# Performance work log

Measured on AMD Instinct MI355X. Metric: run time of the kernel, lower is better.

The kernel has to match this reference:

```python
import jax, jax.numpy as jnp
import numpy as np

B, L, T = 128, 64, 48
E, H, V_SRC, V_TGT = 512, 512, 32000, 32000
NEG = -1e9


def lstm_cell(x, h, c, Wih, Whh, b):
    g = x @ Wih.T + h @ Whh.T + b
    i, f, gg, o = jnp.split(g, 4, axis=-1)
    c2 = jax.nn.sigmoid(f) * c + jax.nn.sigmoid(i) * jnp.tanh(gg)
    return jax.nn.sigmoid(o) * jnp.tanh(c2), c2


def setup_inputs() -> dict:
    key = jax.random.key(0)
    ks = jax.random.split(key, 24)
    s = 0.02
    src_tokens = jax.random.randint(ks[0], (B, L), 0, V_SRC)
    trg_tokens = jax.random.randint(ks[1], (B, T), 0, V_TGT)
    # packed-sequence semantics require descending src_lens; max must equal L
    src_lens = jnp.sort(jax.random.randint(ks[2], (B,), L // 2, L + 1))[::-1].at[0].set(L)
    trg_lens = jnp.sort(jax.random.randint(ks[3], (B,), T // 2, T + 1))[::-1].at[0].set(T)
    p = lambda k, shp: (jax.random.normal(k, shp, dtype=jnp.float32) * s)
    return {
        'src_tokens': src_tokens, 'src_lens': src_lens,
        'trg_tokens': trg_tokens, 'trg_lens': trg_lens,
        'src_emb': p(ks[4], (V_SRC, E)), 'trg_emb': p(ks[5], (V_TGT, E)),
        'enc_Wih0': p(ks[6], (4 * H, E)), 'enc_Whh0': p(ks[7], (4 * H, H)), 'enc_b0': p(ks[8], (4 * H,)),
        'enc_Wih1': p(ks[9], (4 * H, H)), 'enc_Whh1': p(ks[10], (4 * H, H)), 'enc_b1': p(ks[11], (4 * H,)),
        'dec_Wih': p(ks[12], (4 * H, E + H)), 'dec_Whh': p(ks[13], (4 * H, H)), 'dec_b': p(ks[14], (4 * H,)),
        'hid_W': p(ks[15], (H, 2 * H)), 'hid_b': p(ks[16], (H,)),
        'out_W': p(ks[17], (V_TGT, H)), 'out_b': p(ks[18], (V_TGT,)),
        'init_W': p(ks[19], (H, 2 * H)), 'init_b': p(ks[20], (H,)),
    }


def reference(src_tokens, src_lens, trg_tokens, trg_lens,
              src_emb, trg_emb,
              enc_Wih0, enc_Whh0, enc_b0, enc_Wih1, enc_Whh1, enc_b1,
              dec_Wih, dec_Whh, dec_b,
              hid_W, hid_b, out_W, out_b, init_W, init_b):
    # ---- encode (2-layer LSTM with packed-sequence semantics; dropout in eval = identity) ----
    x = src_emb[src_tokens]                                   # (B, L, E)
    xs = jnp.swapaxes(x, 0, 1)                                # (L, B, E)
    step_mask = (jnp.arange(L)[:, None] < src_lens[None, :])[..., None]  # (L, B, 1)
    z = jnp.zeros((B, H), dtype=x.dtype)

    def enc_step(carry, inp):
        h1, c1, h2, c2 = carry
        x_t, m = inp
        nh1, nc1 = lstm_cell(x_t, h1, c1, enc_Wih0, enc_Whh0, enc_b0)
        nh2, nc2 = lstm_cell(nh1, h2, c2, enc_Wih1, enc_Whh1, enc_b1)
        h1 = jnp.where(m, nh1, h1); c1 = jnp.where(m, nc1, c1)
        h2 = jnp.where(m, nh2, h2); c2 = jnp.where(m, nc2, c2)
        return (h1, c1, h2, c2), jnp.where(m, nh2, 0.0)

    (h1, c1, h2, c2), outs = jax.lax.scan(enc_step, (z, z, z, z), (xs, step_mask))
    src_states = jnp.swapaxes(outs, 0, 1)                     # (B, L, H), zero-padded
    final_cell = jnp.concatenate([c1, c2], axis=-1)           # (B, 2H) = layers flattened
    c0 = final_cell @ init_W.T + init_b
    h0 = jnp.tanh(c0)

    # ---- decode (teacher forcing; dot-product attention masked by src_lens) ----
    src_pos_mask = jnp.arange(L)[None, :] < src_lens[:, None]  # (B, L)
    toks = jnp.swapaxes(trg_tokens[:, :-1], 0, 1)              # (T-1, B)
    tgts = jnp.swapaxes(trg_tokens[:, 1:], 0, 1)               # (T-1, B)

    def dec_step(carry, inp):
        h, c, av = carry
        tok, tgt = inp
        v = trg_emb[tok]                                       # (B, E)
        h, c = lstm_cell(jnp.concatenate([v, av], -1), h, c, dec_Wih, dec_Whh, dec_b)
        scores = jnp.einsum('bh,blh->bl', h, src_states)
        scores = jnp.where(src_pos_mask, scores, NEG)
        attn = jax.nn.softmax(scores, axis=-1)
        ctx = jnp.einsum('bl,blh->bh', attn, src_states)
        av = jnp.concatenate([h, ctx], -1) @ hid_W.T + hid_b
        logits = av @ out_W.T + out_b                          # (B, V_TGT)
        logp = jax.nn.log_softmax(logits, axis=-1)
        nll = -jnp.take_along_axis(logp, tgt[:, None], axis=-1)[:, 0]
        return (h, c, av), nll

    _, nll = jax.lax.scan(dec_step, (h0, c0, z), (toks, tgts))
    nll = jnp.swapaxes(nll, 0, 1)                              # (B, T-1)
    mask = (jnp.arange(T)[None, :] < trg_lens[:, None]).astype(nll.dtype)
    return jnp.sum(-nll * mask[:, 1:])
```

## Files before the change

### kernel.cpp

```cpp
#include <hip/hip_runtime.h>
#include <hip/hip_bf16.h>
#include <math.h>

typedef __bf16 bf16;
typedef __bf16 bf16x8 __attribute__((ext_vector_type(8)));
typedef float  f32x4  __attribute__((ext_vector_type(4)));

#define MFMA16(a,b,c) __builtin_amdgcn_mfma_f32_16x16x32_bf16(a,b,c,0,0,0)

namespace {

constexpr int Bn = 128, Ln = 64, Tn = 48, En = 512, Hn = 512, Vn = 32000;
constexpr int G4 = 2048;
constexpr int TD = Tn - 1;
constexpr int MD = TD * Bn;
constexpr float NEGV = -1e9f;
constexpr int HB = Bn * Hn;

__device__ __forceinline__ float sigm(float x){ return 1.f/(1.f+__expf(-x)); }

__global__ void k_conv(const float4* __restrict__ s, ushort4* __restrict__ d, int n4){
  int i = blockIdx.x*256 + threadIdx.x;
  if (i >= n4) return;
  float4 v = s[i];
  union { bf16 h[4]; ushort4 u; } pk;
  pk.h[0]=(bf16)v.x; pk.h[1]=(bf16)v.y; pk.h[2]=(bf16)v.z; pk.h[3]=(bf16)v.w;
  d[i] = pk.u;
}

__global__ void k_gather_src(const int* __restrict__ toks, const float* __restrict__ emb,
                             ushort4* __restrict__ Xe){
  int i = blockIdx.x*256 + threadIdx.x;
  int e4 = i & (En/4 - 1);
  int r  = i >> 7;
  int l = r >> 7, b = r & (Bn-1);
  int tok = toks[b*Ln + l];
  float4 v = *(const float4*)(emb + (size_t)tok*En + e4*4);
  union { bf16 h[4]; ushort4 u; } pk;
  pk.h[0]=(bf16)v.x; pk.h[1]=(bf16)v.y; pk.h[2]=(bf16)v.z; pk.h[3]=(bf16)v.w;
  Xe[i] = pk.u;
}

__global__ void k_gather_trg(const int* __restrict__ toks, const float* __restrict__ emb,
                             ushort4* __restrict__ Vg){
  int i = blockIdx.x*256 + threadIdx.x;
  int e4 = i & (En/4 - 1);
  int r  = i >> 7;
  int t = r >> 7, b = r & (Bn-1);
  int tok = toks[b*Tn + t];
  float4 v = *(const float4*)(emb + (size_t)tok*En + e4*4);
  union { bf16 h[4]; ushort4 u; } pk;
  pk.h[0]=(bf16)v.x; pk.h[1]=(bf16)v.y; pk.h[2]=(bf16)v.z; pk.h[3]=(bf16)v.w;
  Vg[i] = pk.u;
}

__global__ void k_zero(bf16* __restrict__ a, bf16* __restrict__ b,
                       float* __restrict__ c, float* __restrict__ d,
                       float* __restrict__ outp){
  int i = blockIdx.x*256 + threadIdx.x;
  a[i] = (bf16)0.f; b[i] = (bf16)0.f; c[i] = 0.f; d[i] = 0.f;
  if (i == 0) outp[0] = 0.f;
}

template<int MODE>
__global__ void __launch_bounds__(512) k_gemm(
    const bf16* __restrict__ A, const bf16* __restrict__ Bw,
    const float* __restrict__ bias, void* __restrict__ Ovp,
    float* __restrict__ pmax, float* __restrict__ psum,
    int Ncols, int Mrows)
{
  constexpr int K = 512;
  int lane = threadIdx.x & 63, w = threadIdx.x >> 6;
  int wr = w & 3, wc = w >> 2;
  int mt = blockIdx.x, nt = blockIdx.y;
  int mBase = mt*128 + wr*32;
  int nBase = nt*256 + wc*128;
  int laneK = (lane >> 4) * 8;
  const bf16* Ap = A  + (size_t)(mBase + (lane&15))*K + laneK;
  const bf16* Bp = Bw + (size_t)(nBase + (lane&15))*K + laneK;
  f32x4 acc[2][8] = {};
  for (int kb = 0; kb < K; kb += 32){
    bf16x8 a0 = *(const bf16x8*)(Ap + kb);
    bf16x8 a1 = *(const bf16x8*)(Ap + (size_t)16*K + kb);
    #pragma unroll
    for (int fn = 0; fn < 8; ++fn){
      bf16x8 bv = *(const bf16x8*)(Bp + (size_t)fn*16*K + kb);
      acc[0][fn] = MFMA16(a0, bv, acc[0][fn]);
      acc[1][fn] = MFMA16(a1, bv, acc[1][fn]);
    }
  }
  float bvv[8];
  #pragma unroll
  for (int fn = 0; fn < 8; ++fn) bvv[fn] = bias[nBase + fn*16 + (lane&15)];

  if constexpr (MODE == 0){
    bf16* O = (bf16*)Ovp;
    #pragma unroll
    for (int fm = 0; fm < 2; ++fm){
      #pragma unroll
      for (int r = 0; r < 4; ++r){
        size_t ro = (size_t)(mBase + fm*16 + ((lane>>4)<<2) + r) * Ncols;
        #pragma unroll
        for (int fn = 0; fn < 8; ++fn)
          O[ro + nBase + fn*16 + (lane&15)] = (bf16)(acc[fm][fn][r] + bvv[fn]);
      }
    }
  } else {
    int pc = nt*2 + wc;
    #pragma unroll
    for (int fm = 0; fm < 2; ++fm){
      #pragma unroll
      for (int r = 0; r < 4; ++r){
        float mx = -1e30f;
        #pragma unroll
        for (int fn = 0; fn < 8; ++fn) mx = fmaxf(mx, acc[fm][fn][r] + bvv[fn]);
        mx = fmaxf(mx, __shfl_xor(mx, 1));
        mx = fmaxf(mx, __shfl_xor(mx, 2));
        mx = fmaxf(mx, __shfl_xor(mx, 4));
        mx = fmaxf(mx, __shfl_xor(mx, 8));
        float sm = 0.f;
        #pragma unroll
        for (int fn = 0; fn < 8; ++fn) sm += __expf(acc[fm][fn][r] + bvv[fn] - mx);
        sm += __shfl_xor(sm, 1); sm += __shfl_xor(sm, 2);
        sm += __shfl_xor(sm, 4); sm += __shfl_xor(sm, 8);
        if ((lane & 15) == 0){
          int row = mBase + fm*16 + ((lane>>4)<<2) + r;
          pmax[(size_t)pc*Mrows + row] = mx;
          psum[(size_t)pc*Mrows + row] = sm;
        }
      }
    }
  }
}

__device__ __forceinline__ void kloop4(f32x4 acc[4], const bf16* __restrict__ Ap,
                                       const bf16* __restrict__ Wp, int ldw, int col)
{
  for (int kb = 0; kb < 512; kb += 32){
    bf16x8 a = *(const bf16x8*)(Ap + kb);
    #pragma unroll
    for (int q = 0; q < 4; ++q){
      bf16x8 bv = *(const bf16x8*)(Wp + (size_t)(q*Hn + col)*ldw + kb);
      acc[q] = MFMA16(a, bv, acc[q]);
    }
  }
}

__global__ void __launch_bounds__(256) k_enc(
    const bf16* __restrict__ Xg,
    bf16* __restrict__ h1b, bf16* __restrict__ h2b,
    float* __restrict__ c1, float* __restrict__ c2,
    const bf16* __restrict__ Whh0, const bf16* __restrict__ Wih1,
    const bf16* __restrict__ Whh1, const float* __restrict__ b1,
    const int* __restrict__ slens, bf16* __restrict__ Sst, int t)
{
  int bx = blockIdx.x;
  int lane = threadIdx.x & 63, w = threadIdx.x >> 6;
  bool isE2 = bx >= 64;
  int bb = isE2 ? bx - 64 : bx;
  int mt = bb >> 3, cg = bb & 7;
  int col  = cg*64 + w*16 + (lane & 15);
  int rowA = mt*16 + (lane & 15);
  int rowC = mt*16 + ((lane >> 4) << 2);
  int laneK = (lane >> 4) * 8;
  int rb = t & 1;

  if (!isE2){
    if (t >= Ln) return;
    f32x4 acc[4];
    #pragma unroll
    for (int q = 0; q < 4; ++q){
      #pragma unroll
      for (int r = 0; r < 4; ++r)
        acc[q][r] = (float)Xg[((size_t)(t*Bn + rowC + r))*G4 + q*Hn + col];
    }
    kloop4(acc, h1b + rb*HB + rowA*Hn + laneK, Whh0 + laneK, Hn, col);
    #pragma unroll
    for (int r = 0; r < 4; ++r){
      int grow = rowC + r;
      float cold = c1[grow*Hn + col];
      float iv = sigm(acc[0][r]), fv = sigm(acc[1][r]);
      float gv = tanhf(acc[2][r]), ov = sigm(acc[3][r]);
      float cn = fv*cold + iv*gv;
      float hn = ov*tanhf(cn);
      bool m = t < slens[grow];
      float hold = (float)h1b[rb*HB + grow*Hn + col];
      c1[grow*Hn + col] = m ? cn : cold;
      h1b[(rb^1)*HB + grow*Hn + col] = (bf16)(m ? hn : hold);
    }
  } else {
    int t2 = t - 1;
    if (t2 < 0) return;
    f32x4 acc[4];
    #pragma unroll
    for (int q = 0; q < 4; ++q){
      float bq = b1[q*Hn + col];
      #pragma unroll
      for (int r = 0; r < 4; ++r) acc[q][r] = bq;
    }
    kloop4(acc, h1b + rb*HB + rowA*Hn + laneK, Wih1 + laneK, Hn, col);
    kloop4(acc, h2b + rb*HB + rowA*Hn + laneK, Whh1 + laneK, Hn, col);
    #pragma unroll
    for (int r = 0; r < 4; ++r){
      int grow = rowC + r;
      float cold = c2[grow*Hn + col];
      float iv = sigm(acc[0][r]), fv = sigm(acc[1][r]);
      float gv = tanhf(acc[2][r]), ov = sigm(acc[3][r]);
      float cn = fv*cold + iv*gv;
      float hn = ov*tanhf(cn);
      bool m = t2 < slens[grow];
      float hold = (float)h2b[rb*HB + grow*Hn + col];
      c2[grow*Hn + col] = m ? cn : cold;
      h2b[(rb^1)*HB + grow*Hn + col] = (bf16)(m ? hn : hold);
      Sst[((size_t)grow*Ln + t2)*Hn + col] = m ? (bf16)hn : (bf16)0.f;
    }
  }
}

__global__ void k_dec_init(const float* __restrict__ c1, const float* __restrict__ c2,
                           const float* __restrict__ iW, const float* __restrict__ ib,
                           float* __restrict__ cd, bf16* __restrict__ hdb)
{
  int n = blockIdx.x;
  int b = threadIdx.x;
  float s = ib[n];
  const float* w0 = iW + (size_t)n*(2*Hn);
  for (int k = 0; k < Hn; ++k) s += c1[b*Hn + k] * w0[k];
  for (int k = 0; k < Hn; ++k) s += c2[b*Hn + k] * w0[Hn + k];
  cd[b*Hn + n] = s;
  hdb[b*Hn + n] = (bf16)tanhf(s);
}

__global__ void __launch_bounds__(256) k_dec1(
    const bf16* __restrict__ Vg, const bf16* __restrict__ av_all,
    bf16* __restrict__ hdb, float* __restrict__ cd,
    const bf16* __restrict__ Wdih, const bf16* __restrict__ Wdhh,
    const float* __restrict__ db, int t)
{
  int bb = blockIdx.x;
  int lane = threadIdx.x & 63, w = threadIdx.x >> 6;
  int mt = bb >> 3, cg = bb & 7;
  int col  = cg*64 + w*16 + (lane & 15);
  int rowA = mt*16 + (lane & 15);
  int rowC = mt*16 + ((lane >> 4) << 2);
  int laneK = (lane >> 4) * 8;
  int rb = t & 1;
  f32x4 acc[4];
  #pragma unroll
  for (int q = 0; q < 4; ++q){
    float bq = db[q*Hn + col];
    #pragma unroll
    for (int r = 0; r < 4; ++r) acc[q][r] = bq;
  }
  kloop4(acc, Vg + (size_t)t*Bn*En + rowA*En + laneK, Wdih + laneK, En+Hn, col);
  if (t > 0)
    kloop4(acc, av_all + (size_t)(t-1)*HB + rowA*Hn + laneK, Wdih + En + laneK, En+Hn, col);
  kloop4(acc, hdb + rb*HB + rowA*Hn + laneK, Wdhh + laneK, Hn, col);
  #pragma unroll
  for (int r = 0; r < 4; ++r){
    int grow = rowC + r;
    float cold = cd[grow*Hn + col];
    float iv = sigm(acc[0][r]), fv = sigm(acc[1][r]);
    float gv = tanhf(acc[2][r]), ov = sigm(acc[3][r]);
    float cn = fv*cold + iv*gv;
    float hn = ov*tanhf(cn);
    cd[grow*Hn + col] = cn;
    hdb[(rb^1)*HB + grow*Hn + col] = (bf16)hn;
  }
}

__global__ void __launch_bounds__(256) k_attn(
    const bf16* __restrict__ hdb, const bf16* __restrict__ Sst,
    const int* __restrict__ slens, bf16* __restrict__ ctx, int t)
{
  int b = blockIdx.x, tid = threadIdx.x;
  const bf16* h = hdb + ((t&1)^1)*HB + (size_t)b*Hn;
  const bf16* S = Sst + (size_t)b*Ln*Hn;
  __shared__ float sc[Ln];
  __shared__ float at[Ln];
  int l = tid >> 2, kq = tid & 3;
  float s = 0.f;
  {
    const bf16* hp = h + kq*128;
    const bf16* Sp = S + (size_t)l*Hn + kq*128;
    for (int k8 = 0; k8 < 128; k8 += 8){
      bf16x8 hv = *(const bf16x8*)(hp + k8);
      bf16x8 sv = *(const bf16x8*)(Sp + k8);
      #pragma unroll
      for (int j = 0; j < 8; ++j) s += (float)hv[j]*(float)sv[j];
    }
  }
  s += __shfl_xor(s, 1); s += __shfl_xor(s, 2);
  if (kq == 0) sc[l] = (l < slens[b]) ? s : NEGV;
  __syncthreads();
  float mx = -1e30f;
  for (int j = 0; j < Ln; ++j) mx = fmaxf(mx, sc[j]);
  if (tid < Ln) at[tid] = __expf(sc[tid] - mx);
  __syncthreads();
  float den = 0.f;
  for (int j = 0; j < Ln; ++j) den += at[j];
  float inv = 1.f/den;
  for (int kk = tid; kk < Hn; kk += 256){
    float c = 0.f;
    for (int j = 0; j < Ln; ++j) c += at[j]*(float)S[(size_t)j*Hn + kk];
    ctx[(size_t)b*Hn + kk] = (bf16)(c*inv);
  }
}

__global__ void __launch_bounds__(256) k_hid(
    const bf16* __restrict__ hdb, const bf16* __restrict__ ctx,
    const bf16* __restrict__ Whid, const float* __restrict__ hbias,
    bf16* __restrict__ av_all, int t)
{
  int bb = blockIdx.x;
  int lane = threadIdx.x & 63, w = threadIdx.x >> 6;
  int mt = bb >> 3, cg = bb & 7;
  int col  = cg*64 + w*16 + (lane & 15);
  int rowA = mt*16 + (lane & 15);
  int rowC = mt*16 + ((lane >> 4) << 2);
  int laneK = (lane >> 4) * 8;
  int rb2 = (t & 1) ^ 1;
  float bq = hbias[col];
  f32x4 acc = {bq, bq, bq, bq};
  const bf16* Ah = hdb + rb2*HB + rowA*Hn + laneK;
  const bf16* Ac = ctx + rowA*Hn + laneK;
  const bf16* Wp = Whid + (size_t)col*(2*Hn) + laneK;
  for (int kb = 0; kb < 512; kb += 32){
    bf16x8 a  = *(const bf16x8*)(Ah + kb);
    bf16x8 bv = *(const bf16x8*)(Wp + kb);
    acc = MFMA16(a, bv, acc);
  }
  for (int kb = 0; kb < 512; kb += 32){
    bf16x8 a  = *(const bf16x8*)(Ac + kb);
    bf16x8 bv = *(const bf16x8*)(Wp + Hn + kb);
    acc = MFMA16(a, bv, acc);
  }
  #pragma unroll
  for (int r = 0; r < 4; ++r)
    av_all[(size_t)t*HB + (size_t)(rowC + r)*Hn + col] = (bf16)acc[r];
}

__global__ void k_tgt(const bf16* __restrict__ av_all, const bf16* __restrict__ Wout,
                      const float* __restrict__ ob, const int* __restrict__ trg_tokens,
                      float* __restrict__ tlog)
{
  int row = blockIdx.x*4 + (threadIdx.x >> 6);
  int lane = threadIdx.x & 63;
  int t = row >> 7, b = row & 127;
  int tok = trg_tokens[b*Tn + t + 1];
  bf16x8 va = *(const bf16x8*)(av_all + (size_t)row*Hn + lane*8);
  bf16x8 vw = *(const bf16x8*)(Wout + (size_t)tok*Hn + lane*8);
  float s = 0.f;
  #pragma unroll
  for (int j = 0; j < 8; ++j) s += (float)va[j]*(float)vw[j];
  #pragma unroll
  for (int sh = 1; sh < 64; sh <<= 1) s += __shfl_xor(s, sh);
  if (lane == 0) tlog[row] = s + ob[tok];
}

__global__ void k_lse(const float* __restrict__ pmax, const float* __restrict__ psum,
                      const float* __restrict__ tlog, const int* __restrict__ tlens,
                      float* __restrict__ out)
{
  int row = blockIdx.x*512 + threadIdx.x;
  float contrib = 0.f;
  if (row < MD){
    float mx = -1e30f;
    for (int pc = 0; pc < 250; ++pc) mx = fmaxf(mx, pmax[(size_t)pc*MD + row]);
    float s = 0.f;
    for (int pc = 0; pc < 250; ++pc)
      s += psum[(size_t)pc*MD + row] * __expf(pmax[(size_t)pc*MD + row] - mx);
    float lse = mx + __logf(s);
    int t = row >> 7, b = row & 127;
    if (t + 1 < tlens[b]) contrib = tlog[row] - lse;
  }
  #pragma unroll
  for (int sh = 1; sh < 64; sh <<= 1) contrib += __shfl_xor(contrib, sh);
  __shared__ float wsum[8];
  if ((threadIdx.x & 63) == 0) wsum[threadIdx.x >> 6] = contrib;
  __syncthreads();
  if (threadIdx.x == 0){
    float s2 = 0.f;
    for (int i = 0; i < 8; ++i) s2 += wsum[i];
    atomicAdd(out, s2);
  }
}

}

extern "C" void kernel_launch(void* const* d_in, const int* in_sizes, int n_in,
                              void* d_out, int out_size, void* d_ws, size_t ws_size,
                              hipStream_t stream)
{
  (void)in_sizes; (void)n_in; (void)out_size; (void)ws_size;
  const int*   src_tokens = (const int*)  d_in[0];
  const int*   src_lens   = (const int*)  d_in[1];
  const int*   trg_tokens = (const int*)  d_in[2];
  const int*   trg_lens   = (const int*)  d_in[3];
  const float* src_emb    = (const float*)d_in[4];
  const float* trg_emb    = (const float*)d_in[5];
  const float* eWih0 = (const float*)d_in[6];
  const float* eWhh0 = (const float*)d_in[7];
  const float* eb0   = (const float*)d_in[8];
  const float* eWih1 = (const float*)d_in[9];
  const float* eWhh1 = (const float*)d_in[10];
  const float* eb1   = (const float*)d_in[11];
  const float* dWih  = (const float*)d_in[12];
  const float* dWhh  = (const float*)d_in[13];
  const float* db    = (const float*)d_in[14];
  const float* hW    = (const float*)d_in[15];
  const float* hb    = (const float*)d_in[16];
  const float* oW    = (const float*)d_in[17];
  const float* ob    = (const float*)d_in[18];
  const float* iW    = (const float*)d_in[19];
  const float* ib    = (const float*)d_in[20];

  char* p = (char*)d_ws;
  auto alloc = [&](size_t bytes)->void*{
    void* r = (void*)p; p += (bytes + 255) & ~(size_t)255; return r;
  };
  bf16* wih0  = (bf16*)alloc((size_t)G4*En*2);
  bf16* whh0  = (bf16*)alloc((size_t)G4*Hn*2);
  bf16* wih1  = (bf16*)alloc((size_t)G4*Hn*2);
  bf16* whh1  = (bf16*)alloc((size_t)G4*Hn*2);
  bf16* wdih  = (bf16*)alloc((size_t)G4*(En+Hn)*2);
  bf16* wdhh  = (bf16*)alloc((size_t)G4*Hn*2);
  bf16* whid  = (bf16*)alloc((size_t)Hn*(2*Hn)*2);
  bf16* wout  = (bf16*)alloc((size_t)Vn*Hn*2);
  bf16* Xe    = (bf16*)alloc((size_t)Ln*Bn*En*2);
  bf16* Vg    = (bf16*)alloc((size_t)TD*Bn*En*2);
  bf16* Sst   = (bf16*)alloc((size_t)Bn*Ln*Hn*2);
  bf16* h1b   = (bf16*)alloc((size_t)2*HB*2);
  bf16* h2b   = (bf16*)alloc((size_t)2*HB*2);
  bf16* hdb   = (bf16*)alloc((size_t)2*HB*2);
  bf16* ctx   = (bf16*)alloc((size_t)HB*2);
  bf16* avall = (bf16*)alloc((size_t)TD*HB*2);
  bf16* Xg    = (bf16*)alloc((size_t)Ln*Bn*G4*2);
  float* c1   = (float*)alloc((size_t)HB*4);
  float* c2   = (float*)alloc((size_t)HB*4);
  float* cd   = (float*)alloc((size_t)HB*4);
  float* pmax = (float*)alloc((size_t)250*MD*4);
  float* psum = (float*)alloc((size_t)250*MD*4);
  float* tlog = (float*)alloc((size_t)MD*4);
  float* outp = (float*)d_out;

  auto conv = [&](const float* s, bf16* d, int n){
    int n4 = n/4;
    k_conv<<<(n4+255)/256, 256, 0, stream>>>((const float4*)s, (ushort4*)d, n4);
  };
  conv(eWih0, wih0, G4*En);
  conv(eWhh0, whh0, G4*Hn);
  conv(eWih1, wih1, G4*Hn);
  conv(eWhh1, whh1, G4*Hn);
  conv(dWih,  wdih, G4*(En+Hn));
  conv(dWhh,  wdhh, G4*Hn);
  conv(hW,    whid, Hn*2*Hn);
  conv(oW,    wout, Vn*Hn);

  k_gather_src<<<4096, 256, 0, stream>>>(src_tokens, src_emb, (ushort4*)Xe);
  k_gather_trg<<<3008, 256, 0, stream>>>(trg_tokens, trg_emb, (ushort4*)Vg);
  k_zero<<<256, 256, 0, stream>>>(h1b, h2b + HB, c1, c2, outp);

  k_gemm<0><<<dim3(64, 8), 512, 0, stream>>>(Xe, wih0, eb0, Xg, nullptr, nullptr, G4, Ln*Bn);

  for (int t = 0; t <= Ln; ++t)
    k_enc<<<128, 256, 0, stream>>>(Xg, h1b, h2b, c1, c2, whh0, wih1, whh1, eb1,
                                   src_lens, Sst, t);

  k_dec_init<<<512, 128, 0, stream>>>(c1, c2, iW, ib, cd, hdb);

  for (int t = 0; t < TD; ++t){
    k_dec1<<<64, 256, 0, stream>>>(Vg, avall, hdb, cd, wdih, wdhh, db, t);
    k_attn<<<128, 256, 0, stream>>>(hdb, Sst, src_lens, ctx, t);
    k_hid<<<64, 256, 0, stream>>>(hdb, ctx, whid, hb, avall, t);
  }

  k_tgt<<<1504, 256, 0, stream>>>(avall, wout, ob, trg_tokens, tlog);

  k_gemm<1><<<dim3(47, 125), 512, 0, stream>>>(avall, wout, ob, nullptr, pmax, psum, Vn, MD);

  k_lse<<<12, 512, 0, stream>>>(pmax, psum, tlog, trg_lens, outp);
}
```

Before: 5.282 ms.

## Persistent encoder/decoder kernels with global barriers and LDS-tiled GEMM

Replaces the per-timestep kernel launches of the encoder and decoder with two persistent kernels that loop over time and synchronise blocks through per-row-group atomic flag barriers. The recurrent GEMMs are split along K across waves and reduced in LDS, so 256 blocks are active per step instead of 64-128. The decoder's input-embedding projection is hoisted into one batched GEMM before the loop, and decoder init, attention and the hidden projection are folded in. The large GEMMs now stage tiles into swizzled LDS via global_load_lds. The spin barriers depend on all blocks being co-resident and have a timeout break that could silently desynchronise.

```diff
diff --git a/kernel.cpp b/kernel.cpp
--- a/kernel.cpp
+++ b/kernel.cpp
@@ -18,6 +18,29 @@
 constexpr int HB = Bn * Hn;
 
 __device__ __forceinline__ float sigm(float x){ return 1.f/(1.f+__expf(-x)); }
+
+__device__ __forceinline__ void gload16(const bf16* g, bf16* l){
+  __builtin_amdgcn_global_load_lds(
+    (const __attribute__((address_space(1))) void*)g,
+    (__attribute__((address_space(3))) void*)l, 16, 0, 0);
+}
+
+__device__ __forceinline__ void gbar(int* flags, int gbase, int nb, int slot, int s){
+  __builtin_amdgcn_fence(__ATOMIC_RELEASE, "agent");
+  __syncthreads();
+  if (threadIdx.x == 0)
+    __hip_atomic_store(flags + gbase + slot, s, __ATOMIC_RELAXED, __HIP_MEMORY_SCOPE_AGENT);
+  if ((int)threadIdx.x < nb){
+    int lim = 0;
+    while (__hip_atomic_load(flags + gbase + (int)threadIdx.x,
+                             __ATOMIC_RELAXED, __HIP_MEMORY_SCOPE_AGENT) < s){
+      __builtin_amdgcn_s_sleep(1);
+      if (++lim > (1<<18)) break;
+    }
+  }
+  __syncthreads();
+  __builtin_amdgcn_fence(__ATOMIC_ACQUIRE, "agent");
+}
 
 __global__ void k_conv(const float4* __restrict__ s, ushort4* __restrict__ d, int n4){
   int i = blockIdx.x*256 + threadIdx.x;
@@ -54,133 +77,197 @@
   Vg[i] = pk.u;
 }
 
-__global__ void k_zero(bf16* __restrict__ a, bf16* __restrict__ b,
-                       float* __restrict__ c, float* __restrict__ d,
+__global__ void k_zero(bf16* __restrict__ h1b0, bf16* __restrict__ h2b1,
+                       float* __restrict__ c1, float* __restrict__ c2,
+                       int* __restrict__ ef, int* __restrict__ df,
                        float* __restrict__ outp){
   int i = blockIdx.x*256 + threadIdx.x;
-  a[i] = (bf16)0.f; b[i] = (bf16)0.f; c[i] = 0.f; d[i] = 0.f;
+  h1b0[i] = (bf16)0.f; h2b1[i] = (bf16)0.f; c1[i] = 0.f; c2[i] = 0.f;
+  if (i < 256){ ef[i] = 0; df[i] = 0; }
   if (i == 0) outp[0] = 0.f;
 }
 
 template<int MODE>
-__global__ void __launch_bounds__(512) k_gemm(
-    const bf16* __restrict__ A, const bf16* __restrict__ Bw,
-    const float* __restrict__ bias, void* __restrict__ Ovp,
-    float* __restrict__ pmax, float* __restrict__ psum,
-    int Ncols, int Mrows)
+__global__ void __launch_bounds__(256) k_gemm2(
+    const bf16* __restrict__ A, int lda,
+    const bf16* __restrict__ Bw, int ldb,
+    const float* __restrict__ bias,
+    bf16* __restrict__ O, int ldo,
+    float* __restrict__ pmax, float* __restrict__ psum, int Mrows)
 {
-  constexpr int K = 512;
-  int lane = threadIdx.x & 63, w = threadIdx.x >> 6;
-  int wr = w & 3, wc = w >> 2;
-  int mt = blockIdx.x, nt = blockIdx.y;
-  int mBase = mt*128 + wr*32;
-  int nBase = nt*256 + wc*128;
-  int laneK = (lane >> 4) * 8;
-  const bf16* Ap = A  + (size_t)(mBase + (lane&15))*K + laneK;
-  const bf16* Bp = Bw + (size_t)(nBase + (lane&15))*K + laneK;
-  f32x4 acc[2][8] = {};
-  for (int kb = 0; kb < K; kb += 32){
-    bf16x8 a0 = *(const bf16x8*)(Ap + kb);
-    bf16x8 a1 = *(const bf16x8*)(Ap + (size_t)16*K + kb);
+  __shared__ bf16 As[128*64];
+  __shared__ bf16 Bs[128*64];
+  __shared__ float redm[2][64], reds[2][64];
+  int tid = threadIdx.x;
+  int lane = tid & 63, w = tid >> 6;
+  int wr = w & 1, wc = w >> 1;
+  int c15 = lane & 15, hi = lane >> 4;
+  int mBase = blockIdx.x*128, nBase = blockIdx.y*128;
+  int l8 = lane >> 3;
+  int k8 = (lane & 7) ^ l8;
+  int swz = c15 & 7;
+
+  f32x4 acc[4][4] = {};
+  int rA[4], cB[4];
+  #pragma unroll
+  for (int m = 0; m < 4; ++m) rA[m] = (wr*64 + m*16 + c15)*64;
+  #pragma unroll
+  for (int n = 0; n < 4; ++n) cB[n] = (wc*64 + n*16 + c15)*64;
+
+  for (int kt = 0; kt < 8; ++kt){
+    __syncthreads();
     #pragma unroll
-    for (int fn = 0; fn < 8; ++fn){
-      bf16x8 bv = *(const bf16x8*)(Bp + (size_t)fn*16*K + kb);
-      acc[0][fn] = MFMA16(a0, bv, acc[0][fn]);
-      acc[1][fn] = MFMA16(a1, bv, acc[1][fn]);
-    }
-  }
-  float bvv[8];
+    for (int i = 0; i < 4; ++i){
+      int s = i*4 + w;
+      int row = s*8 + l8;
+      gload16(A + (size_t)(mBase+row)*lda + kt*64 + k8*8, As + s*512);
+      gload16(Bw + (size_t)(nBase+row)*ldb + kt*64 + k8*8, Bs + s*512);
+    }
+    __syncthreads();
+    bf16x8 af[4][2], bf[4][2];
+    #pragma unroll
+    for (int m = 0; m < 4; ++m)
+      #pragma unroll
+      for (int j = 0; j < 2; ++j)
+        af[m][j] = *(const bf16x8*)(As + rA[m] + (((j*4+hi) ^ swz) << 3));
+    #pragma unroll
+    for (int n = 0; n < 4; ++n)
+      #pragma unroll
+      for (int j = 0; j < 2; ++j)
+        bf[n][j] = *(const bf16x8*)(Bs + cB[n] + (((j*4+hi) ^ swz) << 3));
+    #pragma unroll
+    for (int m = 0; m < 4; ++m)
+      #pragma unroll
+      for (int n = 0; n < 4; ++n){
+        acc[m][n] = MFMA16(af[m][0], bf[n][0], acc[m][n]);
+        acc[m][n] = MFMA16(af[m][1], bf[n][1], acc[m][n]);
+      }
+  }
+
+  float bvv[4];
   #pragma unroll
-  for (int fn = 0; fn < 8; ++fn) bvv[fn] = bias[nBase + fn*16 + (lane&15)];
+  for (int n = 0; n < 4; ++n) bvv[n] = bias[nBase + wc*64 + n*16 + c15];
 
   if constexpr (MODE == 0){
-    bf16* O = (bf16*)Ovp;
     #pragma unroll
-    for (int fm = 0; fm < 2; ++fm){
+    for (int m = 0; m < 4; ++m)
       #pragma unroll
       for (int r = 0; r < 4; ++r){
-        size_t ro = (size_t)(mBase + fm*16 + ((lane>>4)<<2) + r) * Ncols;
-        #pragma unroll
-        for (int fn = 0; fn < 8; ++fn)
-          O[ro + nBase + fn*16 + (lane&15)] = (bf16)(acc[fm][fn][r] + bvv[fn]);
-      }
-    }
+        size_t ro = (size_t)(mBase + wr*64 + m*16 + hi*4 + r) * ldo + nBase + wc*64;
+        #pragma unroll
+        for (int n = 0; n < 4; ++n)
+          O[ro + n*16 + c15] = (bf16)(acc[m][n][r] + bvv[n]);
+      }
   } else {
-    int pc = nt*2 + wc;
+    float lmx[4][4], lsm[4][4];
     #pragma unroll
-    for (int fm = 0; fm < 2; ++fm){
+    for (int m = 0; m < 4; ++m)
       #pragma unroll
       for (int r = 0; r < 4; ++r){
         float mx = -1e30f;
         #pragma unroll
-        for (int fn = 0; fn < 8; ++fn) mx = fmaxf(mx, acc[fm][fn][r] + bvv[fn]);
-        mx = fmaxf(mx, __shfl_xor(mx, 1));
-        mx = fmaxf(mx, __shfl_xor(mx, 2));
-        mx = fmaxf(mx, __shfl_xor(mx, 4));
-        mx = fmaxf(mx, __shfl_xor(mx, 8));
+        for (int n = 0; n < 4; ++n) mx = fmaxf(mx, acc[m][n][r] + bvv[n]);
+        mx = fmaxf(mx, __shfl_xor(mx,1)); mx = fmaxf(mx, __shfl_xor(mx,2));
+        mx = fmaxf(mx, __shfl_xor(mx,4)); mx = fmaxf(mx, __shfl_xor(mx,8));
         float sm = 0.f;
         #pragma unroll
-        for (int fn = 0; fn < 8; ++fn) sm += __expf(acc[fm][fn][r] + bvv[fn] - mx);
-        sm += __shfl_xor(sm, 1); sm += __shfl_xor(sm, 2);
-        sm += __shfl_xor(sm, 4); sm += __shfl_xor(sm, 8);
-        if ((lane & 15) == 0){
-          int row = mBase + fm*16 + ((lane>>4)<<2) + r;
-          pmax[(size_t)pc*Mrows + row] = mx;
-          psum[(size_t)pc*Mrows + row] = sm;
-        }
-      }
-    }
-  }
-}
-
-__device__ __forceinline__ void kloop4(f32x4 acc[4], const bf16* __restrict__ Ap,
-                                       const bf16* __restrict__ Wp, int ldw, int col)
-{
-  for (int kb = 0; kb < 512; kb += 32){
-    bf16x8 a = *(const bf16x8*)(Ap + kb);
-    #pragma unroll
-    for (int q = 0; q < 4; ++q){
-      bf16x8 bv = *(const bf16x8*)(Wp + (size_t)(q*Hn + col)*ldw + kb);
-      acc[q] = MFMA16(a, bv, acc[q]);
-    }
-  }
-}
-
-__global__ void __launch_bounds__(256) k_enc(
+        for (int n = 0; n < 4; ++n) sm += __expf(acc[m][n][r] + bvv[n] - mx);
+        sm += __shfl_xor(sm,1); sm += __shfl_xor(sm,2);
+        sm += __shfl_xor(sm,4); sm += __shfl_xor(sm,8);
+        lmx[m][r] = mx; lsm[m][r] = sm;
+        if (c15 == 0 && wc == 1){
+          int rs = m*16 + hi*4 + r;
+          redm[wr][rs] = mx; reds[wr][rs] = sm;
+        }
+      }
+    __syncthreads();
+    if (wc == 0 && c15 == 0){
+      int pc = blockIdx.y;
+      #pragma unroll
+      for (int m = 0; m < 4; ++m)
+        #pragma unroll
+        for (int r = 0; r < 4; ++r){
+          int rs = m*16 + hi*4 + r;
+          float m1 = redm[wr][rs], s1 = reds[wr][rs];
+          float M = fmaxf(lmx[m][r], m1);
+          float S = lsm[m][r]*__expf(lmx[m][r]-M) + s1*__expf(m1-M);
+          size_t o = (size_t)pc*Mrows + mBase + wr*64 + rs;
+          pmax[o] = M; psum[o] = S;
+        }
+    }
+  }
+}
+
+__global__ void __launch_bounds__(256) k_encp(
     const bf16* __restrict__ Xg,
     bf16* __restrict__ h1b, bf16* __restrict__ h2b,
     float* __restrict__ c1, float* __restrict__ c2,
     const bf16* __restrict__ Whh0, const bf16* __restrict__ Wih1,
     const bf16* __restrict__ Whh1, const float* __restrict__ b1,
-    const int* __restrict__ slens, bf16* __restrict__ Sst, int t)
+    const int* __restrict__ slens, bf16* __restrict__ Sst,
+    int* __restrict__ flags)
 {
-  int bx = blockIdx.x;
-  int lane = threadIdx.x & 63, w = threadIdx.x >> 6;
-  bool isE2 = bx >= 64;
-  int bb = isE2 ? bx - 64 : bx;
-  int mt = bb >> 3, cg = bb & 7;
-  int col  = cg*64 + w*16 + (lane & 15);
-  int rowA = mt*16 + (lane & 15);
-  int rowC = mt*16 + ((lane >> 4) << 2);
-  int laneK = (lane >> 4) * 8;
-  int rb = t & 1;
-
-  if (!isE2){
-    if (t >= Ln) return;
-    f32x4 acc[4];
-    #pragma unroll
-    for (int q = 0; q < 4; ++q){
-      #pragma unroll
-      for (int r = 0; r < 4; ++r)
-        acc[q][r] = (float)Xg[((size_t)(t*Bn + rowC + r))*G4 + q*Hn + col];
-    }
-    kloop4(acc, h1b + rb*HB + rowA*Hn + laneK, Whh0 + laneK, Hn, col);
-    #pragma unroll
-    for (int r = 0; r < 4; ++r){
-      int grow = rowC + r;
+  __shared__ float red[2][4][64][17];
+  int tid = threadIdx.x;
+  int lane = tid & 63, w = tid >> 6;
+  int c15 = lane & 15, hi = lane >> 4;
+  int rg = blockIdx.x >> 5, cb = blockIdx.x & 31;
+  int col = cb*16 + c15;
+  int rowA = rg*16 + c15;
+
+  for (int t = 0; t <= Ln; ++t){
+    int rb = t & 1;
+    if (t < Ln){
+      f32x4 a0[4] = {};
+      const bf16* ap = h1b + rb*HB + (size_t)rowA*Hn + w*128 + hi*8;
+      const bf16* bp = Whh0 + (size_t)col*Hn + w*128 + hi*8;
+      for (int kb = 0; kb < 4; ++kb){
+        bf16x8 av = *(const bf16x8*)(ap + kb*32);
+        #pragma unroll
+        for (int q = 0; q < 4; ++q){
+          bf16x8 bv = *(const bf16x8*)(bp + (size_t)q*(512*512) + kb*32);
+          a0[q] = MFMA16(av, bv, a0[q]);
+        }
+      }
+      #pragma unroll
+      for (int q = 0; q < 4; ++q)
+        #pragma unroll
+        for (int r = 0; r < 4; ++r) red[0][w][lane][q*4+r] = a0[q][r];
+    }
+    if (t >= 1){
+      f32x4 a1[4] = {};
+      const bf16* ap1 = h1b + rb*HB + (size_t)rowA*Hn + w*128 + hi*8;
+      const bf16* bp1 = Wih1 + (size_t)col*Hn + w*128 + hi*8;
+      const bf16* ap2 = h2b + rb*HB + (size_t)rowA*Hn + w*128 + hi*8;
+      const bf16* bp2 = Whh1 + (size_t)col*Hn + w*128 + hi*8;
+      for (int kb = 0; kb < 4; ++kb){
+        bf16x8 av1 = *(const bf16x8*)(ap1 + kb*32);
+        bf16x8 av2 = *(const bf16x8*)(ap2 + kb*32);
+        #pragma unroll
+        for (int q = 0; q < 4; ++q){
+          bf16x8 bv1 = *(const bf16x8*)(bp1 + (size_t)q*(512*512) + kb*32);
+          bf16x8 bv2 = *(const bf16x8*)(bp2 + (size_t)q*(512*512) + kb*32);
+          a1[q] = MFMA16(av1, bv1, a1[q]);
+          a1[q] = MFMA16(av2, bv2, a1[q]);
+        }
+      }
+      #pragma unroll
+      for (int q = 0; q < 4; ++q)
+        #pragma unroll
+        for (int r = 0; r < 4; ++r) red[1][w][lane][q*4+r] = a1[q][r];
+    }
+    __syncthreads();
+    int grow = rg*16 + hi*4 + w;
+    if (t < Ln){
+      float g4[4];
+      #pragma unroll
+      for (int q = 0; q < 4; ++q)
+        g4[q] = red[0][0][lane][q*4+w] + red[0][1][lane][q*4+w]
+              + red[0][2][lane][q*4+w] + red[0][3][lane][q*4+w]
+              + (float)Xg[((size_t)t*Bn + grow)*G4 + q*Hn + col];
       float cold = c1[grow*Hn + col];
-      float iv = sigm(acc[0][r]), fv = sigm(acc[1][r]);
-      float gv = tanhf(acc[2][r]), ov = sigm(acc[3][r]);
+      float iv = sigm(g4[0]), fv = sigm(g4[1]);
+      float gv = tanhf(g4[2]), ov = sigm(g4[3]);
       float cn = fv*cold + iv*gv;
       float hn = ov*tanhf(cn);
       bool m = t < slens[grow];
@@ -188,24 +275,17 @@
       c1[grow*Hn + col] = m ? cn : cold;
       h1b[(rb^1)*HB + grow*Hn + col] = (bf16)(m ? hn : hold);
     }
-  } else {
-    int t2 = t - 1;
-    if (t2 < 0) return;
-    f32x4 acc[4];
-    #pragma unroll
-    for (int q = 0; q < 4; ++q){
-      float bq = b1[q*Hn + col];
-      #pragma unroll
-      for (int r = 0; r < 4; ++r) acc[q][r] = bq;
-    }
-    kloop4(acc, h1b + rb*HB + rowA*Hn + laneK, Wih1 + laneK, Hn, col);
-    kloop4(acc, h2b + rb*HB + rowA*Hn + laneK, Whh1 + laneK, Hn, col);
-    #pragma unroll
-    for (int r = 0; r < 4; ++r){
-      int grow = rowC + r;
+    if (t >= 1){
+      int t2 = t - 1;
+      float g4[4];
+      #pragma unroll
+      for (int q = 0; q < 4; ++q)
+        g4[q] = red[1][0][lane][q*4+w] + red[1][1][lane][q*4+w]
+              + red[1][2][lane][q*4+w] + red[1][3][lane][q*4+w]
+              + b1[q*Hn + col];
       float cold = c2[grow*Hn + col];
-      float iv = sigm(acc[0][r]), fv = sigm(acc[1][r]);
-      float gv = tanhf(acc[2][r]), ov = sigm(acc[3][r]);
+      float iv = sigm(g4[0]), fv = sigm(g4[1]);
+      float gv = tanhf(g4[2]), ov = sigm(g4[3]);
       float cn = fv*cold + iv*gv;
       float hn = ov*tanhf(cn);
       bool m = t2 < slens[grow];
@@ -214,130 +294,160 @@
       h2b[(rb^1)*HB + grow*Hn + col] = (bf16)(m ? hn : hold);
       Sst[((size_t)grow*Ln + t2)*Hn + col] = m ? (bf16)hn : (bf16)0.f;
     }
-  }
-}
-
-__global__ void k_dec_init(const float* __restrict__ c1, const float* __restrict__ c2,
-                           const float* __restrict__ iW, const float* __restrict__ ib,
-                           float* __restrict__ cd, bf16* __restrict__ hdb)
+    gbar(flags, rg*32, 32, cb, t+1);
+  }
+}
+
+__global__ void __launch_bounds__(256) k_decp(
+    const bf16* __restrict__ Gx, const bf16* __restrict__ avall_c,
+    bf16* __restrict__ avall, bf16* __restrict__ hdb,
+    float* __restrict__ cd, bf16* __restrict__ ctx,
+    const bf16* __restrict__ Sst,
+    const bf16* __restrict__ Wdih, const bf16* __restrict__ Wdhh,
+    const bf16* __restrict__ Whid, const float* __restrict__ hbias,
+    const float* __restrict__ iW, const float* __restrict__ ib,
+    const float* __restrict__ c1, const float* __restrict__ c2,
+    const int* __restrict__ slens, int* __restrict__ flags)
 {
-  int n = blockIdx.x;
-  int b = threadIdx.x;
-  float s = ib[n];
-  const float* w0 = iW + (size_t)n*(2*Hn);
-  for (int k = 0; k < Hn; ++k) s += c1[b*Hn + k] * w0[k];
-  for (int k = 0; k < Hn; ++k) s += c2[b*Hn + k] * w0[Hn + k];
-  cd[b*Hn + n] = s;
-  hdb[b*Hn + n] = (bf16)tanhf(s);
-}
-
-__global__ void __launch_bounds__(256) k_dec1(
-    const bf16* __restrict__ Vg, const bf16* __restrict__ av_all,
-    bf16* __restrict__ hdb, float* __restrict__ cd,
-    const bf16* __restrict__ Wdih, const bf16* __restrict__ Wdhh,
-    const float* __restrict__ db, int t)
-{
-  int bb = blockIdx.x;
-  int lane = threadIdx.x & 63, w = threadIdx.x >> 6;
-  int mt = bb >> 3, cg = bb & 7;
-  int col  = cg*64 + w*16 + (lane & 15);
-  int rowA = mt*16 + (lane & 15);
-  int rowC = mt*16 + ((lane >> 4) << 2);
-  int laneK = (lane >> 4) * 8;
-  int rb = t & 1;
-  f32x4 acc[4];
-  #pragma unroll
-  for (int q = 0; q < 4; ++q){
-    float bq = db[q*Hn + col];
-    #pragma unroll
-    for (int r = 0; r < 4; ++r) acc[q][r] = bq;
-  }
-  kloop4(acc, Vg + (size_t)t*Bn*En + rowA*En + laneK, Wdih + laneK, En+Hn, col);
-  if (t > 0)
-    kloop4(acc, av_all + (size_t)(t-1)*HB + rowA*Hn + laneK, Wdih + En + laneK, En+Hn, col);
-  kloop4(acc, hdb + rb*HB + rowA*Hn + laneK, Wdhh + laneK, Hn, col);
-  #pragma unroll
-  for (int r = 0; r < 4; ++r){
-    int grow = rowC + r;
-    float cold = cd[grow*Hn + col];
-    float iv = sigm(acc[0][r]), fv = sigm(acc[1][r]);
-    float gv = tanhf(acc[2][r]), ov = sigm(acc[3][r]);
-    float cn = fv*cold + iv*gv;
-    float hn = ov*tanhf(cn);
-    cd[grow*Hn + col] = cn;
-    hdb[(rb^1)*HB + grow*Hn + col] = (bf16)hn;
-  }
-}
-
-__global__ void __launch_bounds__(256) k_attn(
-    const bf16* __restrict__ hdb, const bf16* __restrict__ Sst,
-    const int* __restrict__ slens, bf16* __restrict__ ctx, int t)
-{
-  int b = blockIdx.x, tid = threadIdx.x;
-  const bf16* h = hdb + ((t&1)^1)*HB + (size_t)b*Hn;
-  const bf16* S = Sst + (size_t)b*Ln*Hn;
-  __shared__ float sc[Ln];
-  __shared__ float at[Ln];
-  int l = tid >> 2, kq = tid & 3;
-  float s = 0.f;
+  __shared__ float red[4][64][17];
+  __shared__ float sc[Ln], at[Ln];
+  int tid = threadIdx.x;
+  int lane = tid & 63, w = tid >> 6;
+  int c15 = lane & 15, hi = lane >> 4;
+  int rg = blockIdx.x >> 5, cb = blockIdx.x & 31;
+  int col = cb*16 + c15;
+  int rowA = rg*16 + c15;
+
   {
-    const bf16* hp = h + kq*128;
-    const bf16* Sp = S + (size_t)l*Hn + kq*128;
-    for (int k8 = 0; k8 < 128; k8 += 8){
-      bf16x8 hv = *(const bf16x8*)(hp + k8);
-      bf16x8 sv = *(const bf16x8*)(Sp + k8);
-      #pragma unroll
-      for (int j = 0; j < 8; ++j) s += (float)hv[j]*(float)sv[j];
-    }
-  }
-  s += __shfl_xor(s, 1); s += __shfl_xor(s, 2);
-  if (kq == 0) sc[l] = (l < slens[b]) ? s : NEGV;
-  __syncthreads();
-  float mx = -1e30f;
-  for (int j = 0; j < Ln; ++j) mx = fmaxf(mx, sc[j]);
-  if (tid < Ln) at[tid] = __expf(sc[tid] - mx);
-  __syncthreads();
-  float den = 0.f;
-  for (int j = 0; j < Ln; ++j) den += at[j];
-  float inv = 1.f/den;
-  for (int kk = tid; kk < Hn; kk += 256){
-    float c = 0.f;
-    for (int j = 0; j < Ln; ++j) c += at[j]*(float)S[(size_t)j*Hn + kk];
-    ctx[(size_t)b*Hn + kk] = (bf16)(c*inv);
-  }
-}
-
-__global__ void __launch_bounds__(256) k_hid(
-    const bf16* __restrict__ hdb, const bf16* __restrict__ ctx,
-    const bf16* __restrict__ Whid, const float* __restrict__ hbias,
-    bf16* __restrict__ av_all, int t)
-{
-  int bb = blockIdx.x;
-  int lane = threadIdx.x & 63, w = threadIdx.x >> 6;
-  int mt = bb >> 3, cg = bb & 7;
-  int col  = cg*64 + w*16 + (lane & 15);
-  int rowA = mt*16 + (lane & 15);
-  int rowC = mt*16 + ((lane >> 4) << 2);
-  int laneK = (lane >> 4) * 8;
-  int rb2 = (t & 1) ^ 1;
-  float bq = hbias[col];
-  f32x4 acc = {bq, bq, bq, bq};
-  const bf16* Ah = hdb + rb2*HB + rowA*Hn + laneK;
-  const bf16* Ac = ctx + rowA*Hn + laneK;
-  const bf16* Wp = Whid + (size_t)col*(2*Hn) + laneK;
-  for (int kb = 0; kb < 512; kb += 32){
-    bf16x8 a  = *(const bf16x8*)(Ah + kb);
-    bf16x8 bv = *(const bf16x8*)(Wp + kb);
-    acc = MFMA16(a, bv, acc);
-  }
-  for (int kb = 0; kb < 512; kb += 32){
-    bf16x8 a  = *(const bf16x8*)(Ac + kb);
-    bf16x8 bv = *(const bf16x8*)(Wp + Hn + kb);
-    acc = MFMA16(a, bv, acc);
-  }
-  #pragma unroll
-  for (int r = 0; r < 4; ++r)
-    av_all[(size_t)t*HB + (size_t)(rowC + r)*Hn + col] = (bf16)acc[r];
+    int r_l = tid >> 4, c_l = tid & 15;
+    int row = rg*16 + r_l, ic = cb*16 + c_l;
+    const float4* c1v = (const float4*)(c1 + (size_t)row*Hn);
+    const float4* c2v = (const float4*)(c2 + (size_t)row*Hn);
+    const float4* w1 = (const float4*)(iW + (size_t)ic*1024);
+    const float4* w2 = (const float4*)(iW + (size_t)ic*1024 + 512);
+    float s = ib[ic];
+    for (int k = 0; k < 128; ++k){
+      float4 a = c1v[k], b = w1[k];
+      s += a.x*b.x + a.y*b.y + a.z*b.z + a.w*b.w;
+    }
+    for (int k = 0; k < 128; ++k){
+      float4 a = c2v[k], b = w2[k];
+      s += a.x*b.x + a.y*b.y + a.z*b.z + a.w*b.w;
+    }
+    cd[(size_t)row*Hn + ic] = s;
+    hdb[(size_t)row*Hn + ic] = (bf16)tanhf(s);
+  }
+  gbar(flags, rg*32, 32, cb, 1);
+
+  for (int t = 0; t < TD; ++t){
+    int rb = t & 1;
+    int sbase = 2 + t*3;
+    {
+      f32x4 acc[4] = {};
+      if (w < 2){
+        if (t > 0){
+          const bf16* ap = avall_c + ((size_t)(t-1)*Bn + rowA)*Hn + w*256 + hi*8;
+          const bf16* bp = Wdih + (size_t)col*1024 + 512 + w*256 + hi*8;
+          for (int kb = 0; kb < 8; ++kb){
+            bf16x8 av = *(const bf16x8*)(ap + kb*32);
+            #pragma unroll
+            for (int q = 0; q < 4; ++q){
+              bf16x8 bv = *(const bf16x8*)(bp + (size_t)q*(512*1024) + kb*32);
+              acc[q] = MFMA16(av, bv, acc[q]);
+            }
+          }
+        }
+      } else {
+        const bf16* ap = hdb + rb*HB + (size_t)rowA*Hn + (w-2)*256 + hi*8;
+        const bf16* bp = Wdhh + (size_t)col*Hn + (w-2)*256 + hi*8;
+        for (int kb = 0; kb < 8; ++kb){
+          bf16x8 av = *(const bf16x8*)(ap + kb*32);
+          #pragma unroll
+          for (int q = 0; q < 4; ++q){
+            bf16x8 bv = *(const bf16x8*)(bp + (size_t)q*(512*512) + kb*32);
+            acc[q] = MFMA16(av, bv, acc[q]);
+          }
+        }
+      }
+      #pragma unroll
+      for (int q = 0; q < 4; ++q)
+        #pragma unroll
+        for (int r = 0; r < 4; ++r) red[w][lane][q*4+r] = acc[q][r];
+      __syncthreads();
+      int grow = rg*16 + hi*4 + w;
+      float g4[4];
+      #pragma unroll
+      for (int q = 0; q < 4; ++q)
+        g4[q] = red[0][lane][q*4+w] + red[1][lane][q*4+w]
+              + red[2][lane][q*4+w] + red[3][lane][q*4+w]
+              + (float)Gx[((size_t)t*Bn + grow)*G4 + q*Hn + col];
+      float cold = cd[grow*Hn + col];
+      float iv = sigm(g4[0]), fv = sigm(g4[1]);
+      float gv = tanhf(g4[2]), ov = sigm(g4[3]);
+      float cn = fv*cold + iv*gv;
+      float hn = ov*tanhf(cn);
+      cd[grow*Hn + col] = cn;
+      hdb[(rb^1)*HB + grow*Hn + col] = (bf16)hn;
+    }
+    gbar(flags, rg*32, 32, cb, sbase);
+    {
+      int row = rg*16 + (cb >> 1);
+      int half = cb & 1;
+      const bf16* h = hdb + (rb^1)*HB + (size_t)row*Hn;
+      const bf16* S = Sst + (size_t)row*Ln*Hn;
+      int l = tid >> 2, kq = tid & 3;
+      float s = 0.f;
+      {
+        const bf16* hp = h + kq*128;
+        const bf16* Sp = S + (size_t)l*Hn + kq*128;
+        for (int k8v = 0; k8v < 128; k8v += 8){
+          bf16x8 hv = *(const bf16x8*)(hp + k8v);
+          bf16x8 sv = *(const bf16x8*)(Sp + k8v);
+          #pragma unroll
+          for (int j = 0; j < 8; ++j) s += (float)hv[j]*(float)sv[j];
+        }
+      }
+      s += __shfl_xor(s, 1); s += __shfl_xor(s, 2);
+      if (kq == 0) sc[l] = (l < slens[row]) ? s : NEGV;
+      __syncthreads();
+      float mx = -1e30f;
+      for (int j = 0; j < Ln; ++j) mx = fmaxf(mx, sc[j]);
+      if (tid < Ln) at[tid] = __expf(sc[tid] - mx);
+      __syncthreads();
+      float den = 0.f;
+      for (int j = 0; j < Ln; ++j) den += at[j];
+      float inv = 1.f/den;
+      int kk = half*256 + tid;
+      float cacc = 0.f;
+      for (int j = 0; j < Ln; ++j) cacc += at[j]*(float)S[(size_t)j*Hn + kk];
+      ctx[(size_t)row*Hn + kk] = (bf16)(cacc*inv);
+    }
+    gbar(flags, rg*32, 32, cb, sbase+1);
+    {
+      f32x4 acc = {};
+      const bf16* ap; const bf16* bp;
+      if (w < 2){
+        ap = hdb + (rb^1)*HB + (size_t)rowA*Hn + w*256 + hi*8;
+        bp = Whid + (size_t)col*1024 + w*256 + hi*8;
+      } else {
+        ap = ctx + (size_t)rowA*Hn + (w-2)*256 + hi*8;
+        bp = Whid + (size_t)col*1024 + 512 + (w-2)*256 + hi*8;
+      }
+      for (int kb = 0; kb < 8; ++kb){
+        bf16x8 av = *(const bf16x8*)(ap + kb*32);
+        bf16x8 bv = *(const bf16x8*)(bp + kb*32);
+        acc = MFMA16(av, bv, acc);
+      }
+      #pragma unroll
+      for (int r = 0; r < 4; ++r) red[w][lane][r] = acc[r];
+      __syncthreads();
+      int grow = rg*16 + hi*4 + w;
+      float av4 = red[0][lane][w] + red[1][lane][w] + red[2][lane][w] + red[3][lane][w]
+                + hbias[col];
+      avall[((size_t)t*Bn + grow)*Hn + col] = (bf16)av4;
+    }
+    gbar(flags, rg*32, 32, cb, sbase+2);
+  }
 }
 
 __global__ void k_tgt(const bf16* __restrict__ av_all, const bf16* __restrict__ Wout,
@@ -423,9 +533,9 @@
   bf16* whh0  = (bf16*)alloc((size_t)G4*Hn*2);
   bf16* wih1  = (bf16*)alloc((size_t)G4*Hn*2);
   bf16* whh1  = (bf16*)alloc((size_t)G4*Hn*2);
-  bf16* wdih  = (bf16*)alloc((size_t)G4*(En+Hn)*2);
+  bf16* wdih  = (bf16*)alloc((size_t)G4*1024*2);
   bf16* wdhh  = (bf16*)alloc((size_t)G4*Hn*2);
-  bf16* whid  = (bf16*)alloc((size_t)Hn*(2*Hn)*2);
+  bf16* whid  = (bf16*)alloc((size_t)Hn*1024*2);
   bf16* wout  = (bf16*)alloc((size_t)Vn*Hn*2);
   bf16* Xe    = (bf16*)alloc((size_t)Ln*Bn*En*2);
   bf16* Vg    = (bf16*)alloc((size_t)TD*Bn*En*2);
@@ -442,6 +552,8 @@
   float* pmax = (float*)alloc((size_t)250*MD*4);
   float* psum = (float*)alloc((size_t)250*MD*4);
   float* tlog = (float*)alloc((size_t)MD*4);
+  int*   eflg = (int*)alloc(256*4);
+  int*   dflg = (int*)alloc(256*4);
   float* outp = (float*)d_out;
 
   auto conv = [&](const float* s, bf16* d, int n){
@@ -452,32 +564,32 @@
   conv(eWhh0, whh0, G4*Hn);
   conv(eWih1, wih1, G4*Hn);
   conv(eWhh1, whh1, G4*Hn);
-  conv(dWih,  wdih, G4*(En+Hn));
+  conv(dWih,  wdih, G4*1024);
   conv(dWhh,  wdhh, G4*Hn);
-  conv(hW,    whid, Hn*2*Hn);
+  conv(hW,    whid, Hn*1024);
   conv(oW,    wout, Vn*Hn);
 
   k_gather_src<<<4096, 256, 0, stream>>>(src_tokens, src_emb, (ushort4*)Xe);
   k_gather_trg<<<3008, 256, 0, stream>>>(trg_tokens, trg_emb, (ushort4*)Vg);
-  k_zero<<<256, 256, 0, stream>>>(h1b, h2b + HB, c1, c2, outp);
-
-  k_gemm<0><<<dim3(64, 8), 512, 0, stream>>>(Xe, wih0, eb0, Xg, nullptr, nullptr, G4, Ln*Bn);
-
-  for (int t = 0; t <= Ln; ++t)
-    k_enc<<<128, 256, 0, stream>>>(Xg, h1b, h2b, c1, c2, whh0, wih1, whh1, eb1,
-                                   src_lens, Sst, t);
-
-  k_dec_init<<<512, 128, 0, stream>>>(c1, c2, iW, ib, cd, hdb);
-
-  for (int t = 0; t < TD; ++t){
-    k_dec1<<<64, 256, 0, stream>>>(Vg, avall, hdb, cd, wdih, wdhh, db, t);
-    k_attn<<<128, 256, 0, stream>>>(hdb, Sst, src_lens, ctx, t);
-    k_hid<<<64, 256, 0, stream>>>(hdb, ctx, whid, hb, avall, t);
-  }
+  k_zero<<<256, 256, 0, stream>>>(h1b, h2b + HB, c1, c2, eflg, dflg, outp);
+
+  k_gemm2<0><<<dim3(64, 16), 256, 0, stream>>>(Xe, En, wih0, En, eb0,
+                                               Xg, G4, nullptr, nullptr, 0);
+
+  k_encp<<<256, 256, 0, stream>>>(Xg, h1b, h2b, c1, c2, whh0, wih1, whh1, eb1,
+                                  src_lens, Sst, eflg);
+
+  k_gemm2<0><<<dim3(47, 16), 256, 0, stream>>>(Vg, En, wdih, 1024, db,
+                                               Xg, G4, nullptr, nullptr, 0);
+
+  k_decp<<<256, 256, 0, stream>>>(Xg, avall, avall, hdb, cd, ctx, Sst,
+                                  wdih, wdhh, whid, hb, iW, ib, c1, c2,
+                                  src_lens, dflg);
 
   k_tgt<<<1504, 256, 0, stream>>>(avall, wout, ob, trg_tokens, tlog);
 
-  k_gemm<1><<<dim3(47, 125), 512, 0, stream>>>(avall, wout, ob, nullptr, pmax, psum, Vn, MD);
+  k_gemm2<1><<<dim3(47, 250), 256, 0, stream>>>(avall, En, wout, En, ob,
+                                                nullptr, 0, pmax, psum, MD);
 
   k_lse<<<12, 512, 0, stream>>>(pmax, psum, tlog, trg_lens, outp);
 }
```

Result: slower. 6.940 ms (+31.4%).
